# Kernel optimization log

Hardware: AMD Instinct MI355X
Metric: run time of the kernel (lower is better)

The kernel has to match this reference:

```python
import jax, jax.numpy as jnp
import numpy as np

E = 8       # num experts
T = 1024    # num tokens
H = 1024    # hidden dim
I = 1024    # intermediate dim (per gate/up half)


def setup_inputs() -> dict:
    key = jax.random.key(0)
    k1, k2, k3, k4 = jax.random.split(key, 4)
    return {
        "hidden_states": jax.random.normal(k1, (T, H), jnp.float32),
        "router_logits": jax.random.normal(k2, (T, E), jnp.float32),
        # W13 stored pre-transposed as in the module: [E, H, 2*I]
        "W13": jax.random.normal(k3, (E, H, 2 * I), jnp.float32) * 0.02,
        # W2 stored pre-transposed: [E, I, H]
        "W2": jax.random.normal(k4, (E, I, H), jnp.float32) * 0.02,
        "top_k": 2,
    }


def reference(hidden_states, router_logits, W13, W2, top_k):
    num_experts = router_logits.shape[-1]
    # --- routing: topk_softmax (softmax over all experts, then top-k) ---
    probs = jax.nn.softmax(router_logits, axis=-1)            # [T, E]
    w, idx = jax.lax.top_k(probs, top_k)                      # [T, K]
    # renormalize=True path of moe_gather
    w = w / jnp.sum(w, axis=-1, keepdims=True)
    # combine weights per expert: [T, E]
    combine = jnp.sum(jax.nn.one_hot(idx, num_experts, dtype=w.dtype) * w[..., None], axis=1)
    # --- grouped gate-up GEMM + silu_and_mul ---
    h13 = jnp.einsum('th,ehf->tef', hidden_states, W13)       # [T, E, 2I]
    gate, up = jnp.split(h13, 2, axis=-1)                     # each [T, E, I]
    act = jax.nn.silu(gate) * up                              # silu_and_mul
    # --- grouped down GEMM ---
    down = jnp.einsum('tei,eih->teh', act, W2)                # [T, E, H]
    # --- combine (moe_gather) ---
    return jnp.einsum('te,teh->th', combine, down)            # [T, H]
```

## Files before the change

### kernel.cpp

```cpp
#include <hip/hip_runtime.h>
#include <hip/hip_bf16.h>
#include <stdint.h>

#define NE    8
#define NTOK  1024
#define NH    1024
#define NI    1024
#define N13   2048
#define NPAIR 2048

#define P0_ITEMS 7169
#define G1MAX    736
#define G2MAX    624

typedef __attribute__((ext_vector_type(8))) short short8;
typedef __attribute__((ext_vector_type(4))) float f32x4;
typedef unsigned short u16;
typedef unsigned int   u32;

__device__ __forceinline__ u16 f2bf(float x) {
    union { float f; u32 u; } v; v.f = x;
    return (u16)((v.u + 0x7fffu + ((v.u >> 16) & 1u)) >> 16);
}

__device__ __forceinline__ void async_ld16(u16* lds, const u16* g) {
    __builtin_amdgcn_global_load_lds(
        (const __attribute__((address_space(1))) u32*)g,
        (__attribute__((address_space(3))) u32*)lds, 16, 0, 0);
}

__device__ __forceinline__ bool find_tile(
    const int* __restrict__ counts, int tile, int bm, int ntn,
    int& e_o, int& mt_o, int& nt_o, int& cnt_o, int& base_o)
{
    int base = 0;
    #pragma unroll
    for (int e = 0; e < NE; e++) {
        const int cnt = counts[e];
        const int mtiles = (cnt + bm - 1) / bm;
        const int tiles = mtiles * ntn;
        if (tile < tiles) {
            e_o = e; mt_o = tile / ntn; nt_o = tile - (tile / ntn) * ntn;
            cnt_o = cnt; base_o = base; return true;
        }
        tile -= tiles; base += cnt;
    }
    return false;
}

__global__ __launch_bounds__(256) void prep_all_kernel(
    const float* __restrict__ X, const float* __restrict__ logits,
    const float* __restrict__ W13, const float* __restrict__ W2,
    float* __restrict__ out, int* __restrict__ counts,
    int* __restrict__ pair_tok, float* __restrict__ pair_w,
    u16* __restrict__ Xb, u16* __restrict__ W13t, u16* __restrict__ W2t)
{
    __shared__ __align__(16) float Ts[64][65];
    const int tid = threadIdx.x;
    const int b = blockIdx.x;

    if (b == 0) {
        int* s_cnt  = (int*)&Ts[0][0];
        int* s_base = s_cnt + NE;
        if (tid < NE) s_cnt[tid] = 0;
        __syncthreads();
        int eA[4][2]; int slotA[4][2]; float wA[4][2];
        #pragma unroll
        for (int i = 0; i < 4; i++) {
            const int t = tid * 4 + i;
            float l[NE];
            #pragma unroll
            for (int e = 0; e < NE; e++) l[e] = logits[t * NE + e];
            int i0 = 0;
            #pragma unroll
            for (int e = 1; e < NE; e++) if (l[e] > l[i0]) i0 = e;
            int i1 = -1;
            #pragma unroll
            for (int e = 0; e < NE; e++) {
                if (e == i0) continue;
                if (i1 < 0 || l[e] > l[i1]) i1 = e;
            }
            const float e10 = __expf(l[i1] - l[i0]);
            const float inv = 1.0f / (1.0f + e10);
            eA[i][0] = i0; eA[i][1] = i1;
            wA[i][0] = inv; wA[i][1] = e10 * inv;
            slotA[i][0] = atomicAdd(&s_cnt[i0], 1);
            slotA[i][1] = atomicAdd(&s_cnt[i1], 1);
        }
        __syncthreads();
        if (tid == 0) {
            int acc = 0;
            #pragma unroll
            for (int e = 0; e < NE; e++) { s_base[e] = acc; acc += s_cnt[e]; }
        }
        __syncthreads();
        if (tid < NE) counts[tid] = s_cnt[tid];
        #pragma unroll
        for (int i = 0; i < 4; i++) {
            const int t = tid * 4 + i;
            #pragma unroll
            for (int k = 0; k < 2; k++) {
                const int p = s_base[eA[i][k]] + slotA[i][k];
                pair_tok[p] = t;
                pair_w[p]   = wA[i][k];
            }
        }
    } else if (b <= 512) {
        const int i = (b - 1) * 256 + tid;
        const float4* s = (const float4*)X;
        const float4 a = s[2 * i], c = s[2 * i + 1];
        uint4 o;
        o.x = f2bf(a.x) | ((u32)f2bf(a.y) << 16);
        o.y = f2bf(a.z) | ((u32)f2bf(a.w) << 16);
        o.z = f2bf(c.x) | ((u32)f2bf(c.y) << 16);
        o.w = f2bf(c.z) | ((u32)f2bf(c.w) << 16);
        *(uint4*)(Xb + (size_t)i * 8) = o;
    } else if (b <= 1024) {
        const int i = ((b - 513) * 256 + tid) * 8;
        const float4 z = make_float4(0.f, 0.f, 0.f, 0.f);
        *(float4*)(out + i)     = z;
        *(float4*)(out + i + 4) = z;
    } else {
        const int wb = b - 1025;
        const float* src; u16* dst; int K, N, tb;
        if (wb < 4096) { src = W13; dst = W13t; K = NH; N = N13; tb = wb; }
        else           { src = W2;  dst = W2t;  K = NI; N = NH;  tb = wb - 4096; }
        const int ktiles = K >> 6, ntiles = N >> 6;
        const int tpe = ktiles * ntiles;
        const int e = tb / tpe;
        const int rem = tb - e * tpe;
        const int kt = rem / ntiles, nt = rem - (rem / ntiles) * ntiles;
        const float* sb = src + ((size_t)e * K + (size_t)kt * 64) * N + nt * 64;
        #pragma unroll
        for (int i = 0; i < 4; i++) {
            const int idx = tid + i * 256;
            const int r = idx >> 4, c = (idx & 15) << 2;
            const float4 v = *(const float4*)(sb + (size_t)r * N + c);
            Ts[r][c + 0] = v.x; Ts[r][c + 1] = v.y;
            Ts[r][c + 2] = v.z; Ts[r][c + 3] = v.w;
        }
        __syncthreads();
        u16* db = dst + ((size_t)e * N + (size_t)nt * 64) * K + kt * 64;
        #pragma unroll
        for (int i = 0; i < 2; i++) {
            const int u = tid + i * 256;
            const int n = u >> 3, k8 = (u & 7) << 3;
            uint4 o;
            o.x = f2bf(Ts[k8 + 0][n]) | ((u32)f2bf(Ts[k8 + 1][n]) << 16);
            o.y = f2bf(Ts[k8 + 2][n]) | ((u32)f2bf(Ts[k8 + 3][n]) << 16);
            o.z = f2bf(Ts[k8 + 4][n]) | ((u32)f2bf(Ts[k8 + 5][n]) << 16);
            o.w = f2bf(Ts[k8 + 6][n]) | ((u32)f2bf(Ts[k8 + 7][n]) << 16);
            *(uint4*)(db + (size_t)n * K + k8) = o;
        }
    }
}

__global__ __launch_bounds__(256, 2) void gemm1_kernel(
    const u16* __restrict__ Xb, const u16* __restrict__ W13t,
    const int* __restrict__ counts, const int* __restrict__ pair_tok,
    u16* __restrict__ act)
{
    int e, mt, nt, cnt, base;
    if (!find_tile(counts, blockIdx.x, 128, NI / 32, e, mt, nt, cnt, base)) return;

    __shared__ u16 As[2][128 * 32];
    __shared__ u16 Bs[2][64 * 32];

    const int tid = threadIdx.x;
    const int ct  = nt * 32;

    const int m0 = tid >> 2;
    const int sw16 = (((tid & 3) ^ (m0 & 3)) << 3);
    const int t0 = pair_tok[base + min(mt * 128 + m0, cnt - 1)];
    const int t1 = pair_tok[base + min(mt * 128 + 64 + m0, cnt - 1)];
    const u16* ga0 = Xb + (size_t)t0 * NH + sw16;
    const u16* ga1 = Xb + (size_t)t1 * NH + sw16;
    const int wcol = (m0 < 32) ? (ct + m0) : (NI + ct + m0 - 32);
    const u16* gb = W13t + ((size_t)e * N13 + wcol) * 1024 + sw16;

    const int lane = tid & 63, w = tid >> 6;
    const int quad = lane >> 4, lid = lane & 15;
    const int rw = w >> 1, cw = w & 1;
    const int fsw = (quad ^ (lid & 3)) << 3;
    int aoff[4];
    #pragma unroll
    for (int mi = 0; mi < 4; mi++)
        aoff[mi] = (rw * 64 + mi * 16 + lid) * 32 + fsw;
    const int bgoff = (cw * 16 + lid) * 32 + fsw;
    const int buoff = (32 + cw * 16 + lid) * 32 + fsw;

    f32x4 accg[4] = {};
    f32x4 accu[4] = {};

#define ISSUE1(b, k0)                                        \
    {                                                        \
        async_ld16(&As[b][tid * 8],         ga0 + (k0));     \
        async_ld16(&As[b][(tid + 256) * 8], ga1 + (k0));     \
        async_ld16(&Bs[b][tid * 8],         gb  + (k0));     \
    }
#define COMP1(b)                                                               \
    {                                                                          \
        short8 av[4];                                                          \
        _Pragma("unroll") for (int mi = 0; mi < 4; mi++)                       \
            av[mi] = *(const short8*)&As[b][aoff[mi]];                         \
        const short8 gv = *(const short8*)&Bs[b][bgoff];                       \
        const short8 uv = *(const short8*)&Bs[b][buoff];                       \
        _Pragma("unroll") for (int mi = 0; mi < 4; mi++) {                     \
            accg[mi] = __builtin_amdgcn_mfma_f32_16x16x32_bf16(                \
                av[mi], gv, accg[mi], 0, 0, 0);                                \
            accu[mi] = __builtin_amdgcn_mfma_f32_16x16x32_bf16(                \
                av[mi], uv, accu[mi], 0, 0, 0);                                \
        }                                                                      \
    }

    ISSUE1(0, 0);
    int buf = 0;
    for (int k0 = 32; k0 < NH; k0 += 32) {
        __syncthreads();
        ISSUE1(buf ^ 1, k0);
        COMP1(buf);
        buf ^= 1;
    }
    __syncthreads();
    COMP1(buf);

    const int col = ct + cw * 16 + lid;
    #pragma unroll
    for (int mi = 0; mi < 4; mi++) {
        #pragma unroll
        for (int r = 0; r < 4; r++) {
            const int row = mt * 128 + rw * 64 + mi * 16 + quad * 4 + r;
            if (row < cnt) {
                const float g = accg[mi][r], u = accu[mi][r];
                const float s = g / (1.0f + __expf(-g)) * u;
                act[(size_t)(base + row) * NI + col] = f2bf(s);
            }
        }
    }
#undef ISSUE1
#undef COMP1
}

__global__ __launch_bounds__(256, 2) void gemm2_kernel(
    const u16* __restrict__ act, const u16* __restrict__ W2t,
    const int* __restrict__ counts, const int* __restrict__ pair_tok,
    const float* __restrict__ pair_w, float* __restrict__ out)
{
    int e, mt, nt, cnt, base;
    if (!find_tile(counts, blockIdx.x, 64, NH / 64, e, mt, nt, cnt, base)) return;

    __shared__ u16 As[2][64 * 32];
    __shared__ u16 Bs[2][64 * 32];

    const int tid = threadIdx.x;
    const int ct  = nt * 64;

    const int m0 = tid >> 2;
    const int sw16 = (((tid & 3) ^ (m0 & 3)) << 3);
    const int p0 = base + min(mt * 64 + m0, cnt - 1);
    const u16* ga = act + (size_t)p0 * NI + sw16;
    const u16* gb = W2t + ((size_t)e * 1024 + ct + m0) * 1024 + sw16;

    const int lane = tid & 63, w = tid >> 6;
    const int quad = lane >> 4, lid = lane & 15;
    const int rw = w >> 1, cw = w & 1;
    const int fsw = (quad ^ (lid & 3)) << 3;
    int aoff[2], boff[2];
    #pragma unroll
    for (int mi = 0; mi < 2; mi++)
        aoff[mi] = (rw * 32 + mi * 16 + lid) * 32 + fsw;
    #pragma unroll
    for (int nj = 0; nj < 2; nj++)
        boff[nj] = (cw * 32 + nj * 16 + lid) * 32 + fsw;

    f32x4 acc[2][2] = {};

#define ISSUE2(b, k0)                                        \
    {                                                        \
        async_ld16(&As[b][tid * 8], ga + (k0));              \
        async_ld16(&Bs[b][tid * 8], gb + (k0));              \
    }
#define COMP2(b)                                                               \
    {                                                                          \
        short8 av[2], bv[2];                                                   \
        _Pragma("unroll") for (int mi = 0; mi < 2; mi++)                       \
            av[mi] = *(const short8*)&As[b][aoff[mi]];                         \
        _Pragma("unroll") for (int nj = 0; nj < 2; nj++)                       \
            bv[nj] = *(const short8*)&Bs[b][boff[nj]];                         \
        _Pragma("unroll") for (int mi = 0; mi < 2; mi++)                       \
            _Pragma("unroll") for (int nj = 0; nj < 2; nj++)                   \
                acc[mi][nj] = __builtin_amdgcn_mfma_f32_16x16x32_bf16(         \
                    av[mi], bv[nj], acc[mi][nj], 0, 0, 0);                     \
    }

    ISSUE2(0, 0);
    int buf = 0;
    for (int k0 = 32; k0 < NI; k0 += 32) {
        __syncthreads();
        ISSUE2(buf ^ 1, k0);
        COMP2(buf);
        buf ^= 1;
    }
    __syncthreads();
    COMP2(buf);

    #pragma unroll
    for (int mi = 0; mi < 2; mi++) {
        #pragma unroll
        for (int r = 0; r < 4; r++) {
            const int row = mt * 64 + rw * 32 + mi * 16 + quad * 4 + r;
            if (row < cnt) {
                const int p = base + row;
                const int t = pair_tok[p];
                const float wgt = pair_w[p];
                #pragma unroll
                for (int nj = 0; nj < 2; nj++) {
                    const int col = ct + cw * 32 + nj * 16 + lid;
                    atomicAdd(out + (size_t)t * NH + col, wgt * acc[mi][nj][r]);
                }
            }
        }
    }
#undef ISSUE2
#undef COMP2
}

extern "C" void kernel_launch(void* const* d_in, const int* in_sizes, int n_in,
                              void* d_out, int out_size, void* d_ws, size_t ws_size,
                              hipStream_t stream)
{
    const float* X      = (const float*)d_in[0];
    const float* logits = (const float*)d_in[1];
    const float* W13    = (const float*)d_in[2];
    const float* W2     = (const float*)d_in[3];
    float* out = (float*)d_out;

    char* ws = (char*)d_ws;
    int*   counts   = (int*)(ws + 0);
    int*   pair_tok = (int*)(ws + 256);
    float* pair_w   = (float*)(ws + 256 + 8192);
    u16*   Xb       = (u16*)(ws + 65536);
    u16*   W13t     = (u16*)(ws + 4194304);
    u16*   W2t      = (u16*)(ws + 4194304 + 33554432);
    u16*   act      = (u16*)(ws + 54525952);

    prep_all_kernel<<<P0_ITEMS, 256, 0, stream>>>(
        X, logits, W13, W2, out, counts, pair_tok, pair_w, Xb, W13t, W2t);
    gemm1_kernel<<<G1MAX, 256, 0, stream>>>(Xb, W13t, counts, pair_tok, act);
    gemm2_kernel<<<G2MAX, 256, 0, stream>>>(act, W2t, counts, pair_tok, pair_w, out);
}
```

Measured before the change: 180.1 us.

## Fuse weight bf16 conversion into GEMM loads and replace atomics with combine kernel

```diff
diff --git a/kernel.cpp b/kernel.cpp
--- a/kernel.cpp
+++ b/kernel.cpp
@@ -1,5 +1,4 @@
 #include <hip/hip_runtime.h>
-#include <hip/hip_bf16.h>
 #include <stdint.h>
 
 #define NE    8
@@ -7,11 +6,10 @@
 #define NH    1024
 #define NI    1024
 #define N13   2048
-#define NPAIR 2048
-
-#define P0_ITEMS 7169
-#define G1MAX    736
-#define G2MAX    624
+
+#define PREP_BLOCKS 513
+#define G1MAX       512
+#define G2MAX       256
 
 typedef __attribute__((ext_vector_type(8))) short short8;
 typedef __attribute__((ext_vector_type(4))) float f32x4;
@@ -48,20 +46,18 @@
     return false;
 }
 
-__global__ __launch_bounds__(256) void prep_all_kernel(
+__global__ __launch_bounds__(256) void prep_kernel(
     const float* __restrict__ X, const float* __restrict__ logits,
-    const float* __restrict__ W13, const float* __restrict__ W2,
-    float* __restrict__ out, int* __restrict__ counts,
-    int* __restrict__ pair_tok, float* __restrict__ pair_w,
-    u16* __restrict__ Xb, u16* __restrict__ W13t, u16* __restrict__ W2t)
-{
-    __shared__ __align__(16) float Ts[64][65];
+    int* __restrict__ counts, int* __restrict__ pair_tok,
+    int* __restrict__ inv, float* __restrict__ tokw,
+    u16* __restrict__ Xb)
+{
+    __shared__ int s_cnt[NE];
+    __shared__ int s_base[NE];
     const int tid = threadIdx.x;
     const int b = blockIdx.x;
 
     if (b == 0) {
-        int* s_cnt  = (int*)&Ts[0][0];
-        int* s_base = s_cnt + NE;
         if (tid < NE) s_cnt[tid] = 0;
         __syncthreads();
         int eA[4][2]; int slotA[4][2]; float wA[4][2];
@@ -81,9 +77,9 @@
                 if (i1 < 0 || l[e] > l[i1]) i1 = e;
             }
             const float e10 = __expf(l[i1] - l[i0]);
-            const float inv = 1.0f / (1.0f + e10);
+            const float invw = 1.0f / (1.0f + e10);
             eA[i][0] = i0; eA[i][1] = i1;
-            wA[i][0] = inv; wA[i][1] = e10 * inv;
+            wA[i][0] = invw; wA[i][1] = e10 * invw;
             slotA[i][0] = atomicAdd(&s_cnt[i0], 1);
             slotA[i][1] = atomicAdd(&s_cnt[i1], 1);
         }
@@ -102,10 +98,11 @@
             for (int k = 0; k < 2; k++) {
                 const int p = s_base[eA[i][k]] + slotA[i][k];
                 pair_tok[p] = t;
-                pair_w[p]   = wA[i][k];
+                inv[t * 2 + k] = p;
+                tokw[t * 2 + k] = wA[i][k];
             }
         }
-    } else if (b <= 512) {
+    } else {
         const int i = (b - 1) * 256 + tid;
         const float4* s = (const float4*)X;
         const float4 a = s[2 * i], c = s[2 * i + 1];
@@ -115,55 +112,18 @@
         o.z = f2bf(c.x) | ((u32)f2bf(c.y) << 16);
         o.w = f2bf(c.z) | ((u32)f2bf(c.w) << 16);
         *(uint4*)(Xb + (size_t)i * 8) = o;
-    } else if (b <= 1024) {
-        const int i = ((b - 513) * 256 + tid) * 8;
-        const float4 z = make_float4(0.f, 0.f, 0.f, 0.f);
-        *(float4*)(out + i)     = z;
-        *(float4*)(out + i + 4) = z;
-    } else {
-        const int wb = b - 1025;
-        const float* src; u16* dst; int K, N, tb;
-        if (wb < 4096) { src = W13; dst = W13t; K = NH; N = N13; tb = wb; }
-        else           { src = W2;  dst = W2t;  K = NI; N = NH;  tb = wb - 4096; }
-        const int ktiles = K >> 6, ntiles = N >> 6;
-        const int tpe = ktiles * ntiles;
-        const int e = tb / tpe;
-        const int rem = tb - e * tpe;
-        const int kt = rem / ntiles, nt = rem - (rem / ntiles) * ntiles;
-        const float* sb = src + ((size_t)e * K + (size_t)kt * 64) * N + nt * 64;
-        #pragma unroll
-        for (int i = 0; i < 4; i++) {
-            const int idx = tid + i * 256;
-            const int r = idx >> 4, c = (idx & 15) << 2;
-            const float4 v = *(const float4*)(sb + (size_t)r * N + c);
-            Ts[r][c + 0] = v.x; Ts[r][c + 1] = v.y;
-            Ts[r][c + 2] = v.z; Ts[r][c + 3] = v.w;
-        }
-        __syncthreads();
-        u16* db = dst + ((size_t)e * N + (size_t)nt * 64) * K + kt * 64;
-        #pragma unroll
-        for (int i = 0; i < 2; i++) {
-            const int u = tid + i * 256;
-            const int n = u >> 3, k8 = (u & 7) << 3;
-            uint4 o;
-            o.x = f2bf(Ts[k8 + 0][n]) | ((u32)f2bf(Ts[k8 + 1][n]) << 16);
-            o.y = f2bf(Ts[k8 + 2][n]) | ((u32)f2bf(Ts[k8 + 3][n]) << 16);
-            o.z = f2bf(Ts[k8 + 4][n]) | ((u32)f2bf(Ts[k8 + 5][n]) << 16);
-            o.w = f2bf(Ts[k8 + 6][n]) | ((u32)f2bf(Ts[k8 + 7][n]) << 16);
-            *(uint4*)(db + (size_t)n * K + k8) = o;
-        }
     }
 }
 
 __global__ __launch_bounds__(256, 2) void gemm1_kernel(
-    const u16* __restrict__ Xb, const u16* __restrict__ W13t,
+    const u16* __restrict__ Xb, const float* __restrict__ W13,
     const int* __restrict__ counts, const int* __restrict__ pair_tok,
     u16* __restrict__ act)
 {
     int e, mt, nt, cnt, base;
-    if (!find_tile(counts, blockIdx.x, 128, NI / 32, e, mt, nt, cnt, base)) return;
-
-    __shared__ u16 As[2][128 * 32];
+    if (!find_tile(counts, blockIdx.x, 256, NI / 32, e, mt, nt, cnt, base)) return;
+
+    __shared__ u16 As[2][256 * 32];
     __shared__ u16 Bs[2][64 * 32];
 
     const int tid = threadIdx.x;
@@ -171,85 +131,110 @@
 
     const int m0 = tid >> 2;
     const int sw16 = (((tid & 3) ^ (m0 & 3)) << 3);
-    const int t0 = pair_tok[base + min(mt * 128 + m0, cnt - 1)];
-    const int t1 = pair_tok[base + min(mt * 128 + 64 + m0, cnt - 1)];
-    const u16* ga0 = Xb + (size_t)t0 * NH + sw16;
-    const u16* ga1 = Xb + (size_t)t1 * NH + sw16;
-    const int wcol = (m0 < 32) ? (ct + m0) : (NI + ct + m0 - 32);
-    const u16* gb = W13t + ((size_t)e * N13 + wcol) * 1024 + sw16;
+    const u16* ga[4];
+    #pragma unroll
+    for (int i = 0; i < 4; i++) {
+        const int t = pair_tok[base + min(mt * 256 + i * 64 + m0, cnt - 1)];
+        ga[i] = Xb + (size_t)t * NH + sw16;
+    }
+
+    const int kp  = tid & 15;
+    const int ncg = tid >> 4;
+    const int n0  = ncg << 2;
+    const int f0  = (n0 < 32) ? (ct + n0) : (NI + ct + n0 - 32);
+    const float* gw = W13 + ((size_t)e * NH + 2 * kp) * N13 + f0;
 
     const int lane = tid & 63, w = tid >> 6;
     const int quad = lane >> 4, lid = lane & 15;
-    const int rw = w >> 1, cw = w & 1;
     const int fsw = (quad ^ (lid & 3)) << 3;
-    int aoff[4];
+    int aoff[4], boff[4];
     #pragma unroll
     for (int mi = 0; mi < 4; mi++)
-        aoff[mi] = (rw * 64 + mi * 16 + lid) * 32 + fsw;
-    const int bgoff = (cw * 16 + lid) * 32 + fsw;
-    const int buoff = (32 + cw * 16 + lid) * 32 + fsw;
-
-    f32x4 accg[4] = {};
-    f32x4 accu[4] = {};
-
-#define ISSUE1(b, k0)                                        \
-    {                                                        \
-        async_ld16(&As[b][tid * 8],         ga0 + (k0));     \
-        async_ld16(&As[b][(tid + 256) * 8], ga1 + (k0));     \
-        async_ld16(&Bs[b][tid * 8],         gb  + (k0));     \
-    }
+        aoff[mi] = (w * 64 + mi * 16 + lid) * 32 + fsw;
+    #pragma unroll
+    for (int nf = 0; nf < 4; nf++)
+        boff[nf] = (nf * 16 + lid) * 32 + fsw;
+
+    f32x4 accg[4][2] = {};
+    f32x4 accu[4][2] = {};
+
+#define ISSUE1(b, k0)                                                 \
+    { _Pragma("unroll") for (int i = 0; i < 4; i++)                   \
+        async_ld16(&As[b][(tid + i * 256) * 8], ga[i] + (k0)); }
+
+#define WR_B(b, v0, v1)                                                        \
+    { _Pragma("unroll") for (int j = 0; j < 4; j++) {                          \
+        const int n = n0 + j;                                                  \
+        const u32 pv = (u32)f2bf(((const float*)&(v0))[j]) |                   \
+                       ((u32)f2bf(((const float*)&(v1))[j]) << 16);            \
+        *(u32*)&Bs[b][(n << 5) + ((2 * kp) ^ ((n & 3) << 3))] = pv;            \
+    } }
+
 #define COMP1(b)                                                               \
     {                                                                          \
         short8 av[4];                                                          \
         _Pragma("unroll") for (int mi = 0; mi < 4; mi++)                       \
             av[mi] = *(const short8*)&As[b][aoff[mi]];                         \
-        const short8 gv = *(const short8*)&Bs[b][bgoff];                       \
-        const short8 uv = *(const short8*)&Bs[b][buoff];                       \
+        short8 bv[4];                                                          \
+        _Pragma("unroll") for (int nf = 0; nf < 4; nf++)                       \
+            bv[nf] = *(const short8*)&Bs[b][boff[nf]];                         \
         _Pragma("unroll") for (int mi = 0; mi < 4; mi++) {                     \
-            accg[mi] = __builtin_amdgcn_mfma_f32_16x16x32_bf16(                \
-                av[mi], gv, accg[mi], 0, 0, 0);                                \
-            accu[mi] = __builtin_amdgcn_mfma_f32_16x16x32_bf16(                \
-                av[mi], uv, accu[mi], 0, 0, 0);                                \
+            _Pragma("unroll") for (int c = 0; c < 2; c++) {                    \
+                accg[mi][c] = __builtin_amdgcn_mfma_f32_16x16x32_bf16(         \
+                    av[mi], bv[c], accg[mi][c], 0, 0, 0);                      \
+                accu[mi][c] = __builtin_amdgcn_mfma_f32_16x16x32_bf16(         \
+                    av[mi], bv[c + 2], accu[mi][c], 0, 0, 0);                  \
+            }                                                                  \
         }                                                                      \
     }
 
-    ISSUE1(0, 0);
+    {
+        const float4 v0 = *(const float4*)(gw);
+        const float4 v1 = *(const float4*)(gw + N13);
+        ISSUE1(0, 0);
+        WR_B(0, v0, v1);
+    }
     int buf = 0;
     for (int k0 = 32; k0 < NH; k0 += 32) {
         __syncthreads();
+        const float4 v0 = *(const float4*)(gw + (size_t)k0 * N13);
+        const float4 v1 = *(const float4*)(gw + (size_t)k0 * N13 + N13);
         ISSUE1(buf ^ 1, k0);
         COMP1(buf);
+        WR_B(buf ^ 1, v0, v1);
         buf ^= 1;
     }
     __syncthreads();
     COMP1(buf);
 
-    const int col = ct + cw * 16 + lid;
     #pragma unroll
     for (int mi = 0; mi < 4; mi++) {
         #pragma unroll
         for (int r = 0; r < 4; r++) {
-            const int row = mt * 128 + rw * 64 + mi * 16 + quad * 4 + r;
+            const int row = mt * 256 + w * 64 + mi * 16 + quad * 4 + r;
             if (row < cnt) {
-                const float g = accg[mi][r], u = accu[mi][r];
-                const float s = g / (1.0f + __expf(-g)) * u;
-                act[(size_t)(base + row) * NI + col] = f2bf(s);
+                #pragma unroll
+                for (int c = 0; c < 2; c++) {
+                    const float g = accg[mi][c][r], u = accu[mi][c][r];
+                    const float s = g / (1.0f + __expf(-g)) * u;
+                    act[(size_t)(base + row) * NI + ct + c * 16 + lid] = f2bf(s);
+                }
             }
         }
     }
 #undef ISSUE1
+#undef WR_B
 #undef COMP1
 }
 
 __global__ __launch_bounds__(256, 2) void gemm2_kernel(
-    const u16* __restrict__ act, const u16* __restrict__ W2t,
-    const int* __restrict__ counts, const int* __restrict__ pair_tok,
-    const float* __restrict__ pair_w, float* __restrict__ out)
+    const u16* __restrict__ act, const float* __restrict__ W2,
+    const int* __restrict__ counts, float* __restrict__ down)
 {
     int e, mt, nt, cnt, base;
-    if (!find_tile(counts, blockIdx.x, 64, NH / 64, e, mt, nt, cnt, base)) return;
-
-    __shared__ u16 As[2][64 * 32];
+    if (!find_tile(counts, blockIdx.x, 256, NH / 64, e, mt, nt, cnt, base)) return;
+
+    __shared__ u16 As[2][256 * 32];
     __shared__ u16 Bs[2][64 * 32];
 
     const int tid = threadIdx.x;
@@ -257,72 +242,111 @@
 
     const int m0 = tid >> 2;
     const int sw16 = (((tid & 3) ^ (m0 & 3)) << 3);
-    const int p0 = base + min(mt * 64 + m0, cnt - 1);
-    const u16* ga = act + (size_t)p0 * NI + sw16;
-    const u16* gb = W2t + ((size_t)e * 1024 + ct + m0) * 1024 + sw16;
+    const u16* ga[4];
+    #pragma unroll
+    for (int i = 0; i < 4; i++) {
+        const int p = base + min(mt * 256 + i * 64 + m0, cnt - 1);
+        ga[i] = act + (size_t)p * NI + sw16;
+    }
+
+    const int kp  = tid & 15;
+    const int ncg = tid >> 4;
+    const int n0  = ncg << 2;
+    const float* gw = W2 + ((size_t)e * NI + 2 * kp) * NH + ct + n0;
 
     const int lane = tid & 63, w = tid >> 6;
     const int quad = lane >> 4, lid = lane & 15;
-    const int rw = w >> 1, cw = w & 1;
     const int fsw = (quad ^ (lid & 3)) << 3;
-    int aoff[2], boff[2];
-    #pragma unroll
-    for (int mi = 0; mi < 2; mi++)
-        aoff[mi] = (rw * 32 + mi * 16 + lid) * 32 + fsw;
-    #pragma unroll
-    for (int nj = 0; nj < 2; nj++)
-        boff[nj] = (cw * 32 + nj * 16 + lid) * 32 + fsw;
-
-    f32x4 acc[2][2] = {};
-
-#define ISSUE2(b, k0)                                        \
-    {                                                        \
-        async_ld16(&As[b][tid * 8], ga + (k0));              \
-        async_ld16(&Bs[b][tid * 8], gb + (k0));              \
-    }
+    int aoff[4], boff[4];
+    #pragma unroll
+    for (int mi = 0; mi < 4; mi++)
+        aoff[mi] = (w * 64 + mi * 16 + lid) * 32 + fsw;
+    #pragma unroll
+    for (int nj = 0; nj < 4; nj++)
+        boff[nj] = (nj * 16 + lid) * 32 + fsw;
+
+    f32x4 acc[4][4] = {};
+
+#define ISSUE2(b, k0)                                                 \
+    { _Pragma("unroll") for (int i = 0; i < 4; i++)                   \
+        async_ld16(&As[b][(tid + i * 256) * 8], ga[i] + (k0)); }
+
+#define WR_B2(b, v0, v1)                                                       \
+    { _Pragma("unroll") for (int j = 0; j < 4; j++) {                          \
+        const int n = n0 + j;                                                  \
+        const u32 pv = (u32)f2bf(((const float*)&(v0))[j]) |                   \
+                       ((u32)f2bf(((const float*)&(v1))[j]) << 16);            \
+        *(u32*)&Bs[b][(n << 5) + ((2 * kp) ^ ((n & 3) << 3))] = pv;            \
+    } }
+
 #define COMP2(b)                                                               \
     {                                                                          \
-        short8 av[2], bv[2];                                                   \
-        _Pragma("unroll") for (int mi = 0; mi < 2; mi++)                       \
+        short8 av[4];                                                          \
+        _Pragma("unroll") for (int mi = 0; mi < 4; mi++)                       \
             av[mi] = *(const short8*)&As[b][aoff[mi]];                         \
-        _Pragma("unroll") for (int nj = 0; nj < 2; nj++)                       \
+        short8 bv[4];                                                          \
+        _Pragma("unroll") for (int nj = 0; nj < 4; nj++)                       \
             bv[nj] = *(const short8*)&Bs[b][boff[nj]];                         \
-        _Pragma("unroll") for (int mi = 0; mi < 2; mi++)                       \
-            _Pragma("unroll") for (int nj = 0; nj < 2; nj++)                   \
+        _Pragma("unroll") for (int mi = 0; mi < 4; mi++)                       \
+            _Pragma("unroll") for (int nj = 0; nj < 4; nj++)                   \
                 acc[mi][nj] = __builtin_amdgcn_mfma_f32_16x16x32_bf16(         \
                     av[mi], bv[nj], acc[mi][nj], 0, 0, 0);                     \
     }
 
-    ISSUE2(0, 0);
+    {
+        const float4 v0 = *(const float4*)(gw);
+        const float4 v1 = *(const float4*)(gw + NH);
+        ISSUE2(0, 0);
+        WR_B2(0, v0, v1);
+    }
     int buf = 0;
     for (int k0 = 32; k0 < NI; k0 += 32) {
         __syncthreads();
+        const float4 v0 = *(const float4*)(gw + (size_t)k0 * NH);
+        const float4 v1 = *(const float4*)(gw + (size_t)k0 * NH + NH);
         ISSUE2(buf ^ 1, k0);
         COMP2(buf);
+        WR_B2(buf ^ 1, v0, v1);
         buf ^= 1;
     }
     __syncthreads();
     COMP2(buf);
 
     #pragma unroll
-    for (int mi = 0; mi < 2; mi++) {
+    for (int mi = 0; mi < 4; mi++) {
         #pragma unroll
         for (int r = 0; r < 4; r++) {
-            const int row = mt * 64 + rw * 32 + mi * 16 + quad * 4 + r;
+            const int row = mt * 256 + w * 64 + mi * 16 + quad * 4 + r;
             if (row < cnt) {
-                const int p = base + row;
-                const int t = pair_tok[p];
-                const float wgt = pair_w[p];
                 #pragma unroll
-                for (int nj = 0; nj < 2; nj++) {
-                    const int col = ct + cw * 32 + nj * 16 + lid;
-                    atomicAdd(out + (size_t)t * NH + col, wgt * acc[mi][nj][r]);
+                for (int nj = 0; nj < 4; nj++) {
+                    down[(size_t)(base + row) * NH + ct + nj * 16 + lid] =
+                        acc[mi][nj][r];
                 }
             }
         }
     }
 #undef ISSUE2
+#undef WR_B2
 #undef COMP2
+}
+
+__global__ __launch_bounds__(256) void combine_kernel(
+    const float* __restrict__ down, const int* __restrict__ inv,
+    const float* __restrict__ tokw, float* __restrict__ out)
+{
+    const int t = blockIdx.x;
+    const int p0 = inv[2 * t], p1 = inv[2 * t + 1];
+    const float w0 = tokw[2 * t], w1 = tokw[2 * t + 1];
+    const int i = threadIdx.x * 4;
+    const float4 a = *(const float4*)(down + (size_t)p0 * NH + i);
+    const float4 b = *(const float4*)(down + (size_t)p1 * NH + i);
+    float4 o;
+    o.x = w0 * a.x + w1 * b.x;
+    o.y = w0 * a.y + w1 * b.y;
+    o.z = w0 * a.z + w1 * b.z;
+    o.w = w0 * a.w + w1 * b.w;
+    *(float4*)(out + (size_t)t * NH + i) = o;
 }
 
 extern "C" void kernel_launch(void* const* d_in, const int* in_sizes, int n_in,
@@ -338,14 +362,15 @@
     char* ws = (char*)d_ws;
     int*   counts   = (int*)(ws + 0);
     int*   pair_tok = (int*)(ws + 256);
-    float* pair_w   = (float*)(ws + 256 + 8192);
+    int*   inv      = (int*)(ws + 256 + 8192);
+    float* tokw     = (float*)(ws + 256 + 16384);
     u16*   Xb       = (u16*)(ws + 65536);
-    u16*   W13t     = (u16*)(ws + 4194304);
-    u16*   W2t      = (u16*)(ws + 4194304 + 33554432);
-    u16*   act      = (u16*)(ws + 54525952);
-
-    prep_all_kernel<<<P0_ITEMS, 256, 0, stream>>>(
-        X, logits, W13, W2, out, counts, pair_tok, pair_w, Xb, W13t, W2t);
-    gemm1_kernel<<<G1MAX, 256, 0, stream>>>(Xb, W13t, counts, pair_tok, act);
-    gemm2_kernel<<<G2MAX, 256, 0, stream>>>(act, W2t, counts, pair_tok, pair_w, out);
-}
+    u16*   act      = (u16*)(ws + (size_t)4 * 1024 * 1024);
+    float* down     = (float*)(ws + (size_t)8 * 1024 * 1024);
+
+    prep_kernel<<<PREP_BLOCKS, 256, 0, stream>>>(
+        X, logits, counts, pair_tok, inv, tokw, Xb);
+    gemm1_kernel<<<G1MAX, 256, 0, stream>>>(Xb, W13, counts, pair_tok, act);
+    gemm2_kernel<<<G2MAX, 256, 0, stream>>>(act, W2, counts, down);
+    combine_kernel<<<NTOK, 256, 0, stream>>>(down, inv, tokw, out);
+}
```

New measurement: 216.7 us. 1.2x slower.

## Fuse weight fp32-to-bf16 conversion into GEMM B-tile loads and replace atomics with combine

Applied to the files above, without the earlier changes.

```diff
diff --git a/kernel.cpp b/kernel.cpp
--- a/kernel.cpp
+++ b/kernel.cpp
@@ -1,5 +1,4 @@
 #include <hip/hip_runtime.h>
-#include <hip/hip_bf16.h>
 #include <stdint.h>
 
 #define NE    8
@@ -7,11 +6,10 @@
 #define NH    1024
 #define NI    1024
 #define N13   2048
-#define NPAIR 2048
-
-#define P0_ITEMS 7169
-#define G1MAX    736
-#define G2MAX    624
+
+#define PREP_BLOCKS 513
+#define G1MAX       768
+#define G2MAX       768
 
 typedef __attribute__((ext_vector_type(8))) short short8;
 typedef __attribute__((ext_vector_type(4))) float f32x4;
@@ -21,6 +19,10 @@
 __device__ __forceinline__ u16 f2bf(float x) {
     union { float f; u32 u; } v; v.f = x;
     return (u16)((v.u + 0x7fffu + ((v.u >> 16) & 1u)) >> 16);
+}
+
+__device__ __forceinline__ u32 pack2(float a, float b) {
+    return (u32)f2bf(a) | ((u32)f2bf(b) << 16);
 }
 
 __device__ __forceinline__ void async_ld16(u16* lds, const u16* g) {
@@ -48,20 +50,18 @@
     return false;
 }
 
-__global__ __launch_bounds__(256) void prep_all_kernel(
+__global__ __launch_bounds__(256) void prep_kernel(
     const float* __restrict__ X, const float* __restrict__ logits,
-    const float* __restrict__ W13, const float* __restrict__ W2,
-    float* __restrict__ out, int* __restrict__ counts,
-    int* __restrict__ pair_tok, float* __restrict__ pair_w,
-    u16* __restrict__ Xb, u16* __restrict__ W13t, u16* __restrict__ W2t)
-{
-    __shared__ __align__(16) float Ts[64][65];
+    int* __restrict__ counts, int* __restrict__ pair_tok,
+    int* __restrict__ inv, float* __restrict__ tokw,
+    u16* __restrict__ Xb)
+{
+    __shared__ int s_cnt[NE];
+    __shared__ int s_base[NE];
     const int tid = threadIdx.x;
     const int b = blockIdx.x;
 
     if (b == 0) {
-        int* s_cnt  = (int*)&Ts[0][0];
-        int* s_base = s_cnt + NE;
         if (tid < NE) s_cnt[tid] = 0;
         __syncthreads();
         int eA[4][2]; int slotA[4][2]; float wA[4][2];
@@ -81,9 +81,9 @@
                 if (i1 < 0 || l[e] > l[i1]) i1 = e;
             }
             const float e10 = __expf(l[i1] - l[i0]);
-            const float inv = 1.0f / (1.0f + e10);
+            const float invw = 1.0f / (1.0f + e10);
             eA[i][0] = i0; eA[i][1] = i1;
-            wA[i][0] = inv; wA[i][1] = e10 * inv;
+            wA[i][0] = invw; wA[i][1] = e10 * invw;
             slotA[i][0] = atomicAdd(&s_cnt[i0], 1);
             slotA[i][1] = atomicAdd(&s_cnt[i1], 1);
         }
@@ -102,61 +102,25 @@
             for (int k = 0; k < 2; k++) {
                 const int p = s_base[eA[i][k]] + slotA[i][k];
                 pair_tok[p] = t;
-                pair_w[p]   = wA[i][k];
+                inv[t * 2 + k] = p;
+                tokw[t * 2 + k] = wA[i][k];
             }
         }
-    } else if (b <= 512) {
+    } else {
         const int i = (b - 1) * 256 + tid;
         const float4* s = (const float4*)X;
         const float4 a = s[2 * i], c = s[2 * i + 1];
         uint4 o;
-        o.x = f2bf(a.x) | ((u32)f2bf(a.y) << 16);
-        o.y = f2bf(a.z) | ((u32)f2bf(a.w) << 16);
-        o.z = f2bf(c.x) | ((u32)f2bf(c.y) << 16);
-        o.w = f2bf(c.z) | ((u32)f2bf(c.w) << 16);
+        o.x = pack2(a.x, a.y);
+        o.y = pack2(a.z, a.w);
+        o.z = pack2(c.x, c.y);
+        o.w = pack2(c.z, c.w);
         *(uint4*)(Xb + (size_t)i * 8) = o;
-    } else if (b <= 1024) {
-        const int i = ((b - 513) * 256 + tid) * 8;
-        const float4 z = make_float4(0.f, 0.f, 0.f, 0.f);
-        *(float4*)(out + i)     = z;
-        *(float4*)(out + i + 4) = z;
-    } else {
-        const int wb = b - 1025;
-        const float* src; u16* dst; int K, N, tb;
-        if (wb < 4096) { src = W13; dst = W13t; K = NH; N = N13; tb = wb; }
-        else           { src = W2;  dst = W2t;  K = NI; N = NH;  tb = wb - 4096; }
-        const int ktiles = K >> 6, ntiles = N >> 6;
-        const int tpe = ktiles * ntiles;
-        const int e = tb / tpe;
-        const int rem = tb - e * tpe;
-        const int kt = rem / ntiles, nt = rem - (rem / ntiles) * ntiles;
-        const float* sb = src + ((size_t)e * K + (size_t)kt * 64) * N + nt * 64;
-        #pragma unroll
-        for (int i = 0; i < 4; i++) {
-            const int idx = tid + i * 256;
-            const int r = idx >> 4, c = (idx & 15) << 2;
-            const float4 v = *(const float4*)(sb + (size_t)r * N + c);
-            Ts[r][c + 0] = v.x; Ts[r][c + 1] = v.y;
-            Ts[r][c + 2] = v.z; Ts[r][c + 3] = v.w;
-        }
-        __syncthreads();
-        u16* db = dst + ((size_t)e * N + (size_t)nt * 64) * K + kt * 64;
-        #pragma unroll
-        for (int i = 0; i < 2; i++) {
-            const int u = tid + i * 256;
-            const int n = u >> 3, k8 = (u & 7) << 3;
-            uint4 o;
-            o.x = f2bf(Ts[k8 + 0][n]) | ((u32)f2bf(Ts[k8 + 1][n]) << 16);
-            o.y = f2bf(Ts[k8 + 2][n]) | ((u32)f2bf(Ts[k8 + 3][n]) << 16);
-            o.z = f2bf(Ts[k8 + 4][n]) | ((u32)f2bf(Ts[k8 + 5][n]) << 16);
-            o.w = f2bf(Ts[k8 + 6][n]) | ((u32)f2bf(Ts[k8 + 7][n]) << 16);
-            *(uint4*)(db + (size_t)n * K + k8) = o;
-        }
-    }
-}
-
-__global__ __launch_bounds__(256, 2) void gemm1_kernel(
-    const u16* __restrict__ Xb, const u16* __restrict__ W13t,
+    }
+}
+
+__global__ __launch_bounds__(256, 3) void gemm1_kernel(
+    const u16* __restrict__ Xb, const float* __restrict__ W13,
     const int* __restrict__ counts, const int* __restrict__ pair_tok,
     u16* __restrict__ act)
 {
@@ -170,18 +134,22 @@
     const int ct  = nt * 32;
 
     const int m0 = tid >> 2;
-    const int sw16 = (((tid & 3) ^ (m0 & 3)) << 3);
+    const int sw16 = (((tid & 3) ^ ((tid >> 4) & 3)) << 3);
     const int t0 = pair_tok[base + min(mt * 128 + m0, cnt - 1)];
     const int t1 = pair_tok[base + min(mt * 128 + 64 + m0, cnt - 1)];
     const u16* ga0 = Xb + (size_t)t0 * NH + sw16;
     const u16* ga1 = Xb + (size_t)t1 * NH + sw16;
-    const int wcol = (m0 < 32) ? (ct + m0) : (NI + ct + m0 - 32);
-    const u16* gb = W13t + ((size_t)e * N13 + wcol) * 1024 + sw16;
+
+    const int n0 = (tid & 15) << 2;
+    const int kp = tid >> 4;
+    const int f0 = (n0 < 32) ? (ct + n0) : (NI + ct + n0 - 32);
+    const float* gw = W13 + ((size_t)e * NH + 2 * kp) * N13 + f0;
+    const int bwr = (((kp >> 2) ^ (tid & 3)) << 3) + ((kp & 3) << 1);
 
     const int lane = tid & 63, w = tid >> 6;
     const int quad = lane >> 4, lid = lane & 15;
     const int rw = w >> 1, cw = w & 1;
-    const int fsw = (quad ^ (lid & 3)) << 3;
+    const int fsw = ((quad ^ ((lid >> 2) & 3)) << 3);
     int aoff[4];
     #pragma unroll
     for (int mi = 0; mi < 4; mi++)
@@ -196,7 +164,19 @@
     {                                                        \
         async_ld16(&As[b][tid * 8],         ga0 + (k0));     \
         async_ld16(&As[b][(tid + 256) * 8], ga1 + (k0));     \
-        async_ld16(&Bs[b][tid * 8],         gb  + (k0));     \
+    }
+#define LOADB1(P0, P1, k0)                                            \
+    {                                                                 \
+        P0 = *(const float4*)(gw + (size_t)(k0) * N13);               \
+        P1 = *(const float4*)(gw + (size_t)(k0) * N13 + N13);         \
+    }
+#define WRB1(b, P0, P1)                                               \
+    {                                                                 \
+        u32* d = (u32*)&Bs[b][(n0 << 5) + bwr];                       \
+        d[0]  = pack2(P0.x, P1.x);                                    \
+        d[16] = pack2(P0.y, P1.y);                                    \
+        d[32] = pack2(P0.z, P1.z);                                    \
+        d[48] = pack2(P0.w, P1.w);                                    \
     }
 #define COMP1(b)                                                               \
     {                                                                          \
@@ -213,12 +193,19 @@
         }                                                                      \
     }
 
+    float4 p0, p1, q0, q1;
+    LOADB1(q0, q1, 0);
     ISSUE1(0, 0);
+    WRB1(0, q0, q1);
+    LOADB1(q0, q1, 32);
     int buf = 0;
     for (int k0 = 32; k0 < NH; k0 += 32) {
         __syncthreads();
+        if (k0 + 32 < NH) LOADB1(p0, p1, k0 + 32);
         ISSUE1(buf ^ 1, k0);
         COMP1(buf);
+        WRB1(buf ^ 1, q0, q1);
+        q0 = p0; q1 = p1;
         buf ^= 1;
     }
     __syncthreads();
@@ -238,91 +225,143 @@
         }
     }
 #undef ISSUE1
+#undef LOADB1
+#undef WRB1
 #undef COMP1
 }
 
-__global__ __launch_bounds__(256, 2) void gemm2_kernel(
-    const u16* __restrict__ act, const u16* __restrict__ W2t,
-    const int* __restrict__ counts, const int* __restrict__ pair_tok,
-    const float* __restrict__ pair_w, float* __restrict__ out)
-{
-    int e, mt, nt, cnt, base;
-    if (!find_tile(counts, blockIdx.x, 64, NH / 64, e, mt, nt, cnt, base)) return;
-
-    __shared__ u16 As[2][64 * 32];
+__global__ __launch_bounds__(256, 3) void gemm2_kernel(
+    const u16* __restrict__ act, const float* __restrict__ W2,
+    const int* __restrict__ counts,
+    float* __restrict__ down0, float* __restrict__ down1)
+{
+    int e, mt, ntq, cnt, base;
+    if (!find_tile(counts, blockIdx.x, 128, (NH / 64) * 2, e, mt, ntq, cnt, base)) return;
+    const int kh = ntq & 1;
+    const int nt = ntq >> 1;
+    const int ct = nt * 64;
+    const int kbase = kh * 512;
+    float* __restrict__ dwn = kh ? down1 : down0;
+
+    __shared__ u16 As[2][128 * 32];
     __shared__ u16 Bs[2][64 * 32];
 
     const int tid = threadIdx.x;
-    const int ct  = nt * 64;
 
     const int m0 = tid >> 2;
-    const int sw16 = (((tid & 3) ^ (m0 & 3)) << 3);
-    const int p0 = base + min(mt * 64 + m0, cnt - 1);
-    const u16* ga = act + (size_t)p0 * NI + sw16;
-    const u16* gb = W2t + ((size_t)e * 1024 + ct + m0) * 1024 + sw16;
+    const int sw16 = (((tid & 3) ^ ((tid >> 4) & 3)) << 3);
+    const int p0r = base + min(mt * 128 + m0, cnt - 1);
+    const int p1r = base + min(mt * 128 + 64 + m0, cnt - 1);
+    const u16* ga0 = act + (size_t)p0r * NI + kbase + sw16;
+    const u16* ga1 = act + (size_t)p1r * NI + kbase + sw16;
+
+    const int n0 = (tid & 15) << 2;
+    const int kp = tid >> 4;
+    const float* gw = W2 + ((size_t)e * NI + kbase + 2 * kp) * NH + ct + n0;
+    const int bwr = (((kp >> 2) ^ (tid & 3)) << 3) + ((kp & 3) << 1);
 
     const int lane = tid & 63, w = tid >> 6;
     const int quad = lane >> 4, lid = lane & 15;
     const int rw = w >> 1, cw = w & 1;
-    const int fsw = (quad ^ (lid & 3)) << 3;
-    int aoff[2], boff[2];
-    #pragma unroll
-    for (int mi = 0; mi < 2; mi++)
-        aoff[mi] = (rw * 32 + mi * 16 + lid) * 32 + fsw;
+    const int fsw = ((quad ^ ((lid >> 2) & 3)) << 3);
+    int aoff[4], boff[2];
+    #pragma unroll
+    for (int mi = 0; mi < 4; mi++)
+        aoff[mi] = (rw * 64 + mi * 16 + lid) * 32 + fsw;
     #pragma unroll
     for (int nj = 0; nj < 2; nj++)
         boff[nj] = (cw * 32 + nj * 16 + lid) * 32 + fsw;
 
-    f32x4 acc[2][2] = {};
+    f32x4 acc[4][2] = {};
 
 #define ISSUE2(b, k0)                                        \
     {                                                        \
-        async_ld16(&As[b][tid * 8], ga + (k0));              \
-        async_ld16(&Bs[b][tid * 8], gb + (k0));              \
+        async_ld16(&As[b][tid * 8],         ga0 + (k0));     \
+        async_ld16(&As[b][(tid + 256) * 8], ga1 + (k0));     \
+    }
+#define LOADB2(P0, P1, k0)                                            \
+    {                                                                 \
+        P0 = *(const float4*)(gw + (size_t)(k0) * NH);                \
+        P1 = *(const float4*)(gw + (size_t)(k0) * NH + NH);           \
+    }
+#define WRB2(b, P0, P1)                                               \
+    {                                                                 \
+        u32* d = (u32*)&Bs[b][(n0 << 5) + bwr];                       \
+        d[0]  = pack2(P0.x, P1.x);                                    \
+        d[16] = pack2(P0.y, P1.y);                                    \
+        d[32] = pack2(P0.z, P1.z);                                    \
+        d[48] = pack2(P0.w, P1.w);                                    \
     }
 #define COMP2(b)                                                               \
     {                                                                          \
-        short8 av[2], bv[2];                                                   \
-        _Pragma("unroll") for (int mi = 0; mi < 2; mi++)                       \
+        short8 av[4], bv[2];                                                   \
+        _Pragma("unroll") for (int mi = 0; mi < 4; mi++)                       \
             av[mi] = *(const short8*)&As[b][aoff[mi]];                         \
         _Pragma("unroll") for (int nj = 0; nj < 2; nj++)                       \
             bv[nj] = *(const short8*)&Bs[b][boff[nj]];                         \
-        _Pragma("unroll") for (int mi = 0; mi < 2; mi++)                       \
+        _Pragma("unroll") for (int mi = 0; mi < 4; mi++)                       \
             _Pragma("unroll") for (int nj = 0; nj < 2; nj++)                   \
                 acc[mi][nj] = __builtin_amdgcn_mfma_f32_16x16x32_bf16(         \
                     av[mi], bv[nj], acc[mi][nj], 0, 0, 0);                     \
     }
 
+    float4 p0, p1, q0, q1;
+    LOADB2(q0, q1, 0);
     ISSUE2(0, 0);
+    WRB2(0, q0, q1);
+    LOADB2(q0, q1, 32);
     int buf = 0;
-    for (int k0 = 32; k0 < NI; k0 += 32) {
-        __syncthreads();
+    for (int k0 = 32; k0 < 512; k0 += 32) {
+        __syncthreads();
+        if (k0 + 32 < 512) LOADB2(p0, p1, k0 + 32);
         ISSUE2(buf ^ 1, k0);
         COMP2(buf);
+        WRB2(buf ^ 1, q0, q1);
+        q0 = p0; q1 = p1;
         buf ^= 1;
     }
     __syncthreads();
     COMP2(buf);
 
     #pragma unroll
-    for (int mi = 0; mi < 2; mi++) {
+    for (int mi = 0; mi < 4; mi++) {
         #pragma unroll
         for (int r = 0; r < 4; r++) {
-            const int row = mt * 64 + rw * 32 + mi * 16 + quad * 4 + r;
+            const int row = mt * 128 + rw * 64 + mi * 16 + quad * 4 + r;
             if (row < cnt) {
-                const int p = base + row;
-                const int t = pair_tok[p];
-                const float wgt = pair_w[p];
                 #pragma unroll
                 for (int nj = 0; nj < 2; nj++) {
-                    const int col = ct + cw * 32 + nj * 16 + lid;
-                    atomicAdd(out + (size_t)t * NH + col, wgt * acc[mi][nj][r]);
+                    dwn[(size_t)(base + row) * NH + ct + cw * 32 + nj * 16 + lid] =
+                        acc[mi][nj][r];
                 }
             }
         }
     }
 #undef ISSUE2
+#undef LOADB2
+#undef WRB2
 #undef COMP2
+}
+
+__global__ __launch_bounds__(256) void combine_kernel(
+    const float* __restrict__ down0, const float* __restrict__ down1,
+    const int* __restrict__ inv, const float* __restrict__ tokw,
+    float* __restrict__ out)
+{
+    const int t = blockIdx.x;
+    const int p0 = inv[2 * t], p1 = inv[2 * t + 1];
+    const float w0 = tokw[2 * t], w1 = tokw[2 * t + 1];
+    const int i = threadIdx.x * 4;
+    const float4 a0 = *(const float4*)(down0 + (size_t)p0 * NH + i);
+    const float4 a1 = *(const float4*)(down1 + (size_t)p0 * NH + i);
+    const float4 b0 = *(const float4*)(down0 + (size_t)p1 * NH + i);
+    const float4 b1 = *(const float4*)(down1 + (size_t)p1 * NH + i);
+    float4 o;
+    o.x = w0 * (a0.x + a1.x) + w1 * (b0.x + b1.x);
+    o.y = w0 * (a0.y + a1.y) + w1 * (b0.y + b1.y);
+    o.z = w0 * (a0.z + a1.z) + w1 * (b0.z + b1.z);
+    o.w = w0 * (a0.w + a1.w) + w1 * (b0.w + b1.w);
+    *(float4*)(out + (size_t)t * NH + i) = o;
 }
 
 extern "C" void kernel_launch(void* const* d_in, const int* in_sizes, int n_in,
@@ -337,15 +376,17 @@
 
     char* ws = (char*)d_ws;
     int*   counts   = (int*)(ws + 0);
-    int*   pair_tok = (int*)(ws + 256);
-    float* pair_w   = (float*)(ws + 256 + 8192);
+    int*   pair_tok = (int*)(ws + 1024);
+    int*   inv      = (int*)(ws + 16384);
+    float* tokw     = (float*)(ws + 32768);
     u16*   Xb       = (u16*)(ws + 65536);
-    u16*   W13t     = (u16*)(ws + 4194304);
-    u16*   W2t      = (u16*)(ws + 4194304 + 33554432);
-    u16*   act      = (u16*)(ws + 54525952);
-
-    prep_all_kernel<<<P0_ITEMS, 256, 0, stream>>>(
-        X, logits, W13, W2, out, counts, pair_tok, pair_w, Xb, W13t, W2t);
-    gemm1_kernel<<<G1MAX, 256, 0, stream>>>(Xb, W13t, counts, pair_tok, act);
-    gemm2_kernel<<<G2MAX, 256, 0, stream>>>(act, W2t, counts, pair_tok, pair_w, out);
-}
+    u16*   act      = (u16*)(ws + (size_t)4  * 1024 * 1024);
+    float* down0    = (float*)(ws + (size_t)8  * 1024 * 1024);
+    float* down1    = (float*)(ws + (size_t)16 * 1024 * 1024);
+
+    prep_kernel<<<PREP_BLOCKS, 256, 0, stream>>>(
+        X, logits, counts, pair_tok, inv, tokw, Xb);
+    gemm1_kernel<<<G1MAX, 256, 0, stream>>>(Xb, W13, counts, pair_tok, act);
+    gemm2_kernel<<<G2MAX, 256, 0, stream>>>(act, W2, counts, down0, down1);
+    combine_kernel<<<NTOK, 256, 0, stream>>>(down0, down1, inv, tokw, out);
+}
```

Result: slower. 186.8 us (+3.7%).
